# Kernel tuning notes

Measured on AMD Instinct MI355X. Metric: run time of the kernel, lower is better.

The kernel has to match this reference:

```python
import jax, jax.numpy as jnp
import numpy as np
from jax import lax

B, T, I, H = 32, 512, 512, 1024


def setup_inputs() -> dict:
    key = jax.random.key(0)
    k0, k1, k2, k3, k4 = jax.random.split(key, 5)
    s_i = 1.0 / np.sqrt(I).astype(np.float32)
    s_h = 1.0 / np.sqrt(H).astype(np.float32)
    x = jax.random.normal(k0, (B, T, I), dtype=jnp.float32)
    # stacked gate weights, order: input(i), forget(f), cell(g), output(o)
    Wx = jax.random.uniform(k1, (4 * H, I), jnp.float32, -s_i, s_i)
    bx = jax.random.uniform(k2, (4 * H,), jnp.float32, -s_i, s_i)
    Wh = jax.random.uniform(k3, (4 * H, H), jnp.float32, -s_h, s_h)
    bh = jax.random.uniform(k4, (4 * H,), jnp.float32, -s_h, s_h)
    return {"x": x, "Wx": Wx, "bx": bx, "Wh": Wh, "bh": bh}


def reference(x, Wx, bx, Wh, bh):
    # Pre-compute all input-to-gate projections in one batched GEMM: [B,T,4H]
    xg = jnp.einsum("bti,gi->btg", x, Wx) + bx + bh

    def step(carry, xg_t):
        h, c = carry
        gates = xg_t + h @ Wh.T  # [B,4H]
        i, f, g, o = jnp.split(gates, 4, axis=-1)
        i = jax.nn.sigmoid(i)
        f = jax.nn.sigmoid(f)
        g = jnp.tanh(g)
        o = jax.nn.sigmoid(o)
        c = f * c + i * g
        h = o * jnp.tanh(c)  # r is None in forward -> h_tilde = tanh(c)
        return (h, c), h

    b = x.shape[0]
    h0 = jnp.zeros((b, H), dtype=x.dtype)
    c0 = jnp.zeros((b, H), dtype=x.dtype)
    _, hs = lax.scan(step, (h0, c0), jnp.swapaxes(xg, 0, 1))  # hs: [T,B,H]
    return jnp.swapaxes(hs, 0, 1)  # [B,T,H]
```

## Files before the change

kernel.cpp:

```cpp
#include <hip/hip_runtime.h>
#include <hip/hip_bf16.h>

#define Bv 32
#define Tv 512
#define Iv 512
#define Hv 1024
#define NG 4096

typedef short bf16x8 __attribute__((ext_vector_type(8)));
typedef float floatx16 __attribute__((ext_vector_type(16)));
typedef unsigned short u16;
typedef unsigned long long u64;

__device__ __forceinline__ u16 f2bf(float f) {
  __hip_bfloat16 h = __float2bfloat16(f);
  return *reinterpret_cast<u16*>(&h);
}

__device__ __forceinline__ floatx16 mfma32(bf16x8 a, bf16x8 b, floatx16 c) {
  return __builtin_amdgcn_mfma_f32_32x32x16_bf16(a, b, c, 0, 0, 0);
}

__device__ __forceinline__ u64 ld_agent_u64(const u64* p) {
  return __hip_atomic_load(p, __ATOMIC_RELAXED, __HIP_MEMORY_SCOPE_AGENT);
}
__device__ __forceinline__ void st_agent_u16(u16* p, u16 v) {
  __hip_atomic_store(p, v, __ATOMIC_RELAXED, __HIP_MEMORY_SCOPE_AGENT);
}

__device__ __forceinline__ bf16x8 mk_frag(u64 lo, u64 hi) {
  union { u64 q[2]; bf16x8 v; } u;
  u.q[0] = lo; u.q[1] = hi;
  return u.v;
}

__global__ void k_init(unsigned int* p, int n) {
  int i = blockIdx.x * blockDim.x + threadIdx.x;
  if (i < n) p[i] = 0u;
}

__global__ void k_f2bf(const float* __restrict__ in, u16* __restrict__ out, int n) {
  int i = blockIdx.x * blockDim.x + threadIdx.x;
  if (i < n) out[i] = f2bf(in[i]);
}

__global__ void k_whf(const float* __restrict__ Wh, u16* __restrict__ whf) {
  int tid = blockIdx.x * 256 + threadIdx.x;
  int lane = tid & 63;
  int kt   = (tid >> 6) & 63;
  int nt   = (tid >> 12) & 1;
  int bl   = tid >> 13;
  int r    = nt * 32 + (lane & 31);
  int gate = r >> 4, du = r & 15;
  int row  = gate * Hv + bl * 16 + du;
  int k0   = kt * 16 + (lane >> 5) * 8;
  const float* s = Wh + (size_t)row * Hv + k0;
  u16* d = whf + (size_t)tid * 8;
#pragma unroll
  for (int j = 0; j < 8; ++j) d[j] = f2bf(s[j]);
}

__global__ __launch_bounds__(256) void k_xg(const u16* __restrict__ xb, const u16* __restrict__ wxb,
                                            const float* __restrict__ bx, const float* __restrict__ bh,
                                            float* __restrict__ xg, int t0, int tcshift) {
  __shared__ u16 Al[128 * 40];
  __shared__ u16 Bl[128 * 40];
  int tid = threadIdx.x;
  int wave = tid >> 6, lane = tid & 63;
  int wm = wave & 1, wn = wave >> 1;
  int bm = blockIdx.x, bn = blockIdx.y;
  int Tc = 1 << tcshift;

  floatx16 acc[2][2];
#pragma unroll
  for (int a = 0; a < 2; ++a)
#pragma unroll
    for (int c = 0; c < 2; ++c)
#pragma unroll
      for (int r = 0; r < 16; ++r) acc[a][c][r] = 0.f;

  int lr = tid >> 1;
  int lk = (tid & 1) * 16;
  int m  = bm * 128 + lr;
  int b  = m >> tcshift;
  int tl = m & (Tc - 1);
  const u16* asrc = xb + (size_t)(b * Tv + t0 + tl) * Iv + lk;
  int nrow = bn * 128 + lr;
  const u16* bsrc = wxb + (size_t)nrow * Iv + lk;
  u16* adst = &Al[lr * 40 + lk];
  u16* bdst = &Bl[lr * 40 + lk];

  for (int k0 = 0; k0 < Iv; k0 += 32) {
    __syncthreads();
    *(uint4*)adst       = *(const uint4*)(asrc);
    *(uint4*)(adst + 8) = *(const uint4*)(asrc + 8);
    *(uint4*)bdst       = *(const uint4*)(bsrc);
    *(uint4*)(bdst + 8) = *(const uint4*)(bsrc + 8);
    asrc += 32; bsrc += 32;
    __syncthreads();
#pragma unroll
    for (int kt = 0; kt < 2; ++kt) {
      int ko = kt * 16 + (lane >> 5) * 8;
      bf16x8 a0 = *(const bf16x8*)(&Al[(wm * 64 +      (lane & 31)) * 40 + ko]);
      bf16x8 a1 = *(const bf16x8*)(&Al[(wm * 64 + 32 + (lane & 31)) * 40 + ko]);
      bf16x8 b0 = *(const bf16x8*)(&Bl[(wn * 64 +      (lane & 31)) * 40 + ko]);
      bf16x8 b1 = *(const bf16x8*)(&Bl[(wn * 64 + 32 + (lane & 31)) * 40 + ko]);
      acc[0][0] = mfma32(a0, b0, acc[0][0]);
      acc[0][1] = mfma32(a0, b1, acc[0][1]);
      acc[1][0] = mfma32(a1, b0, acc[1][0]);
      acc[1][1] = mfma32(a1, b1, acc[1][1]);
    }
  }
#pragma unroll
  for (int mt = 0; mt < 2; ++mt) {
#pragma unroll
    for (int ntt = 0; ntt < 2; ++ntt) {
      int nGl = bn * 128 + wn * 64 + ntt * 32 + (lane & 31);
      float bias = bx[nGl] + bh[nGl];
#pragma unroll
      for (int r = 0; r < 16; ++r) {
        int mrow = (r & 3) + 8 * (r >> 2) + 4 * (lane >> 5);
        int mG = bm * 128 + wm * 64 + mt * 32 + mrow;
        int bb = mG >> tcshift;
        int tt = mG & (Tc - 1);
        xg[((size_t)(tt * Bv + bb) << 12) + nGl] = acc[mt][ntt][r] + bias;
      }
    }
  }
}

__global__ __launch_bounds__(256, 1) void k_scan(const u16* __restrict__ whf, const float* __restrict__ xg,
                                                 u64* __restrict__ hA, float* __restrict__ cbuf,
                                                 float* __restrict__ out, int* arrivals, int t0, int Tc) {
  __shared__ float red[4][64][36];
  int tid = threadIdx.x;
  int bl = blockIdx.x;
  int kh = tid >> 6, lane = tid & 63;
  int eu = tid & 15, eb = tid >> 4;
  int u0 = bl * 16;

  bf16x8 w0[16], w1[16];
  {
    const u16* wb0 = whf + ((size_t)(bl * 2 + 0) << 15);
    const u16* wb1 = whf + ((size_t)(bl * 2 + 1) << 15);
#pragma unroll
    for (int kk = 0; kk < 16; ++kk) {
      int kt = kh * 16 + kk;
      w0[kk] = *(const bf16x8*)(wb0 + (size_t)((kt << 6) + lane) * 8);
      w1[kk] = *(const bf16x8*)(wb1 + (size_t)((kt << 6) + lane) * 8);
    }
  }

  float c0, c1;
  if (t0 == 0) { c0 = 0.f; c1 = 0.f; }
  else {
    c0 = cbuf[eb * Hv + u0 + eu];
    c1 = cbuf[(eb + 16) * Hv + u0 + eu];
  }

  u16* hA16 = (u16*)hA;

  float xgv[4][2];
#pragma unroll
  for (int g = 0; g < 4; ++g)
#pragma unroll
    for (int b2 = 0; b2 < 2; ++b2)
      xgv[g][b2] = xg[((size_t)(0 * Bv + eb + 16 * b2) << 12) + g * Hv + u0 + eu];

  for (int tl = 0; tl < Tc; ++tl) {
    int t = t0 + tl;
    const u64* hAr = hA + (size_t)(t & 1) * 8192;

    u64 alo[16], ahi[16];
#pragma unroll
    for (int kk = 0; kk < 16; ++kk) {
      size_t fi = (size_t)((((kh << 4) + kk) << 6) + lane) * 2;
      alo[kk] = ld_agent_u64(hAr + fi);
      ahi[kk] = ld_agent_u64(hAr + fi + 1);
    }

    floatx16 acc0, acc1;
#pragma unroll
    for (int r = 0; r < 16; ++r) { acc0[r] = 0.f; acc1[r] = 0.f; }
#pragma unroll
    for (int kk = 0; kk < 16; ++kk) {
      bf16x8 a = mk_frag(alo[kk], ahi[kk]);
      acc0 = mfma32(a, w0[kk], acc0);
      acc1 = mfma32(a, w1[kk], acc1);
    }

    {
      int n = lane & 31;
      int bq = 4 * (lane >> 5);
#pragma unroll
      for (int rq = 0; rq < 4; ++rq) {
        float4 v0 = make_float4(acc0[rq * 4 + 0], acc0[rq * 4 + 1], acc0[rq * 4 + 2], acc0[rq * 4 + 3]);
        float4 v1 = make_float4(acc1[rq * 4 + 0], acc1[rq * 4 + 1], acc1[rq * 4 + 2], acc1[rq * 4 + 3]);
        *(float4*)&red[kh][n][8 * rq + bq]      = v0;
        *(float4*)&red[kh][32 + n][8 * rq + bq] = v1;
      }
    }

    __syncthreads();

    float hv0, hv1;
    {
      float gs[4][2];
#pragma unroll
      for (int g = 0; g < 4; ++g) {
        int r = g * 16 + eu;
#pragma unroll
        for (int b2 = 0; b2 < 2; ++b2) {
          int b = eb + 16 * b2;
          gs[g][b2] = red[0][r][b] + red[1][r][b] + red[2][r][b] + red[3][r][b] + xgv[g][b2];
        }
      }
      float i0 = 1.f / (1.f + __expf(-gs[0][0]));
      float f0 = 1.f / (1.f + __expf(-gs[1][0]));
      float g0 = 1.f - 2.f / (__expf(2.f * gs[2][0]) + 1.f);
      float o0 = 1.f / (1.f + __expf(-gs[3][0]));
      c0 = f0 * c0 + i0 * g0;
      hv0 = o0 * (1.f - 2.f / (__expf(2.f * c0) + 1.f));

      float i1 = 1.f / (1.f + __expf(-gs[0][1]));
      float f1 = 1.f / (1.f + __expf(-gs[1][1]));
      float g1 = 1.f - 2.f / (__expf(2.f * gs[2][1]) + 1.f);
      float o1 = 1.f / (1.f + __expf(-gs[3][1]));
      c1 = f1 * c1 + i1 * g1;
      hv1 = o1 * (1.f - 2.f / (__expf(2.f * c1) + 1.f));
    }

    u16* hAw16 = hA16 + (size_t)((t + 1) & 1) * 32768;
    st_agent_u16(hAw16 + ((size_t)((bl << 6) + eb +      ((eu >> 3) << 5)) << 3) + (eu & 7), f2bf(hv0));
    st_agent_u16(hAw16 + ((size_t)((bl << 6) + eb + 16 + ((eu >> 3) << 5)) << 3) + (eu & 7), f2bf(hv1));
    asm volatile("s_waitcnt vmcnt(0)" ::: "memory");
    __syncthreads();

    if (tid == 0)
      __hip_atomic_store(arrivals + bl * 16, t + 1, __ATOMIC_RELAXED, __HIP_MEMORY_SCOPE_AGENT);

    out[((size_t)(eb * Tv + t) << 10) + u0 + eu] = hv0;
    out[((size_t)((eb + 16) * Tv + t) << 10) + u0 + eu] = hv1;
    {
      int tln = (tl + 1 < Tc) ? tl + 1 : tl;
#pragma unroll
      for (int g = 0; g < 4; ++g)
#pragma unroll
        for (int b2 = 0; b2 < 2; ++b2)
          xgv[g][b2] = xg[((size_t)(tln * Bv + eb + 16 * b2) << 12) + g * Hv + u0 + eu];
    }

    if (tl + 1 < Tc) {
      if (tid < 64) {
        const int* ap = arrivals + tid * 16;
        while (__hip_atomic_load(ap, __ATOMIC_RELAXED, __HIP_MEMORY_SCOPE_AGENT) < t + 1) { }
      }
      __syncthreads();
    }
  }
  cbuf[eb * Hv + u0 + eu] = c0;
  cbuf[(eb + 16) * Hv + u0 + eu] = c1;
}

extern "C" void kernel_launch(void* const* d_in, const int* in_sizes, int n_in,
                              void* d_out, int out_size, void* d_ws, size_t ws_size,
                              hipStream_t stream) {
  const float* x  = (const float*)d_in[0];
  const float* Wx = (const float*)d_in[1];
  const float* bx = (const float*)d_in[2];
  const float* Wh = (const float*)d_in[3];
  const float* bh = (const float*)d_in[4];
  float* out = (float*)d_out;
  char* ws = (char*)d_ws;

  int*   arrivals = (int*)ws;
  u64*   hA  = (u64*)(ws + 4096);
  float* cb  = (float*)(ws + 4096 + (128 << 10));
  u16*   xb  = (u16*)(ws + 4096 + (256 << 10));
  u16*   wxb = xb + (size_t)Bv * Tv * Iv;
  u16*   whf = wxb + (size_t)NG * Iv;
  float* xg  = (float*)(whf + (size_t)64 * 2 * 64 * 64 * 8);

  size_t fixedB = 4096 + (256ull << 10) +
                  ((size_t)Bv * Tv * Iv + (size_t)NG * Iv + (size_t)64 * 2 * 64 * 64 * 8) * 2;
  int tcshift = 9;
  while (tcshift > 2 && fixedB + (((size_t)Bv * NG * 4) << tcshift) > ws_size) --tcshift;
  int Tc = 1 << tcshift;

  k_init<<<132, 256, 0, stream>>>((unsigned int*)ws, (4096 + (128 << 10)) / 4);
  k_f2bf<<<(Bv * Tv * Iv) / 256, 256, 0, stream>>>(x, xb, Bv * Tv * Iv);
  k_f2bf<<<(NG * Iv) / 256, 256, 0, stream>>>(Wx, wxb, NG * Iv);
  k_whf<<<2048, 256, 0, stream>>>(Wh, whf);

  for (int t0 = 0; t0 < Tv; t0 += Tc) {
    k_xg<<<dim3(Tc / 4, 32), 256, 0, stream>>>(xb, wxb, bx, bh, xg, t0, tcshift);
    k_scan<<<64, 256, 0, stream>>>(whf, xg, hA, cb, out, arrivals, t0, Tc);
  }
}
```

Measured before the change: 2.527 ms.

## Split spin-wait per wave, double-buffer reduction LDS, batch output stores

```diff
diff --git a/kernel.cpp b/kernel.cpp
--- a/kernel.cpp
+++ b/kernel.cpp
@@ -132,7 +132,8 @@
 __global__ __launch_bounds__(256, 1) void k_scan(const u16* __restrict__ whf, const float* __restrict__ xg,
                                                  u64* __restrict__ hA, float* __restrict__ cbuf,
                                                  float* __restrict__ out, int* arrivals, int t0, int Tc) {
-  __shared__ float red[4][64][36];
+  __shared__ float red[2][4][64][36];
+  __shared__ float obuf[16][2][16][16];
   int tid = threadIdx.x;
   int bl = blockIdx.x;
   int kh = tid >> 6, lane = tid & 63;
@@ -159,6 +160,7 @@
   }
 
   u16* hA16 = (u16*)hA;
+  const int* fp = arrivals + ((kh << 4) + (lane & 15)) * 16;
 
   float xgv[4][2];
 #pragma unroll
@@ -169,6 +171,10 @@
 
   for (int tl = 0; tl < Tc; ++tl) {
     int t = t0 + tl;
+
+    while (__hip_atomic_load(fp, __ATOMIC_RELAXED, __HIP_MEMORY_SCOPE_AGENT) < t) { }
+    asm volatile("" ::: "memory");
+
     const u64* hAr = hA + (size_t)(t & 1) * 8192;
 
     u64 alo[16], ahi[16];
@@ -179,6 +185,16 @@
       ahi[kk] = ld_agent_u64(hAr + fi + 1);
     }
 
+    float xgn[4][2];
+    {
+      int tln = (tl + 1 < Tc) ? tl + 1 : tl;
+#pragma unroll
+      for (int g = 0; g < 4; ++g)
+#pragma unroll
+        for (int b2 = 0; b2 < 2; ++b2)
+          xgn[g][b2] = xg[((size_t)(tln * Bv + eb + 16 * b2) << 12) + g * Hv + u0 + eu];
+    }
+
     floatx16 acc0, acc1;
 #pragma unroll
     for (int r = 0; r < 16; ++r) { acc0[r] = 0.f; acc1[r] = 0.f; }
@@ -196,8 +212,8 @@
       for (int rq = 0; rq < 4; ++rq) {
         float4 v0 = make_float4(acc0[rq * 4 + 0], acc0[rq * 4 + 1], acc0[rq * 4 + 2], acc0[rq * 4 + 3]);
         float4 v1 = make_float4(acc1[rq * 4 + 0], acc1[rq * 4 + 1], acc1[rq * 4 + 2], acc1[rq * 4 + 3]);
-        *(float4*)&red[kh][n][8 * rq + bq]      = v0;
-        *(float4*)&red[kh][32 + n][8 * rq + bq] = v1;
+        *(float4*)&red[t & 1][kh][n][8 * rq + bq]      = v0;
+        *(float4*)&red[t & 1][kh][32 + n][8 * rq + bq] = v1;
       }
     }
 
@@ -212,7 +228,8 @@
 #pragma unroll
         for (int b2 = 0; b2 < 2; ++b2) {
           int b = eb + 16 * b2;
-          gs[g][b2] = red[0][r][b] + red[1][r][b] + red[2][r][b] + red[3][r][b] + xgv[g][b2];
+          gs[g][b2] = red[t & 1][0][r][b] + red[t & 1][1][r][b] +
+                      red[t & 1][2][r][b] + red[t & 1][3][r][b] + xgv[g][b2];
         }
       }
       float i0 = 1.f / (1.f + __expf(-gs[0][0]));
@@ -230,6 +247,12 @@
       hv1 = o1 * (1.f - 2.f / (__expf(2.f * c1) + 1.f));
     }
 
+    {
+      int ts = tl & 15;
+      obuf[ts][0][eb][eu] = hv0;
+      obuf[ts][1][eb][eu] = hv1;
+    }
+
     u16* hAw16 = hA16 + (size_t)((t + 1) & 1) * 32768;
     st_agent_u16(hAw16 + ((size_t)((bl << 6) + eb +      ((eu >> 3) << 5)) << 3) + (eu & 7), f2bf(hv0));
     st_agent_u16(hAw16 + ((size_t)((bl << 6) + eb + 16 + ((eu >> 3) << 5)) << 3) + (eu & 7), f2bf(hv1));
@@ -239,24 +262,19 @@
     if (tid == 0)
       __hip_atomic_store(arrivals + bl * 16, t + 1, __ATOMIC_RELAXED, __HIP_MEMORY_SCOPE_AGENT);
 
-    out[((size_t)(eb * Tv + t) << 10) + u0 + eu] = hv0;
-    out[((size_t)((eb + 16) * Tv + t) << 10) + u0 + eu] = hv1;
-    {
-      int tln = (tl + 1 < Tc) ? tl + 1 : tl;
-#pragma unroll
-      for (int g = 0; g < 4; ++g)
-#pragma unroll
-        for (int b2 = 0; b2 < 2; ++b2)
-          xgv[g][b2] = xg[((size_t)(tln * Bv + eb + 16 * b2) << 12) + g * Hv + u0 + eu];
-    }
-
-    if (tl + 1 < Tc) {
-      if (tid < 64) {
-        const int* ap = arrivals + tid * 16;
-        while (__hip_atomic_load(ap, __ATOMIC_RELAXED, __HIP_MEMORY_SCOPE_AGENT) < t + 1) { }
+    if ((tl & 15) == 15 || tl == Tc - 1) {
+      int ns = (tl & 15) + 1;
+      int tb = t - (tl & 15);
+      for (int ts = 0; ts < ns; ++ts) {
+        out[((size_t)(eb * Tv + tb + ts) << 10) + u0 + eu]        = obuf[ts][0][eb][eu];
+        out[((size_t)((eb + 16) * Tv + tb + ts) << 10) + u0 + eu] = obuf[ts][1][eb][eu];
       }
-      __syncthreads();
-    }
+    }
+
+#pragma unroll
+    for (int g = 0; g < 4; ++g)
+#pragma unroll
+      for (int b2 = 0; b2 < 2; ++b2) xgv[g][b2] = xgn[g][b2];
   }
   cbuf[eb * Hv + u0 + eu] = c0;
   cbuf[(eb + 16) * Hv + u0 + eu] = c1;
```

Result: faster. 2.391 ms (-5.4%).
